# Optimization experiments

Hardware: AMD Instinct MI355X
Metric: run time of the kernel (lower is better)

## Reference

```python
import jax, jax.numpy as jnp
import numpy as np

N, E, G = 50000, 800000, 64          # nodes, edges, graphs in batch
H, C = 4, 32                          # heads, per-head channels
D = H * C                             # 128 = gat_hidden_dim * n_heads
EMB = 16
IN_DIM = 2 * EMB + 1                  # 33
LSTM_H = 256
OUT = 4
V_LAB, V_TYP = 1000, 100
EPS = 1e-5


def _gatv2(x, src, dst, Wl, bl, Wr, br, att, bias):
    # GATv2Conv (PyG semantics, self-loops already appended to src/dst).
    xl = (x @ Wl + bl).reshape(-1, H, C)   # lin_l -> source-side messages x_j
    xr = (x @ Wr + br).reshape(-1, H, C)   # lin_r -> target-side x_i
    xj = xl[src]                            # [Et, H, C]
    e = jax.nn.leaky_relu(xr[dst] + xj, 0.2)
    score = jnp.einsum('ehc,hc->eh', e, att)             # [Et, H]
    smax = jax.ops.segment_max(score, dst, num_segments=N)
    a = jnp.exp(score - smax[dst])
    denom = jax.ops.segment_sum(a, dst, num_segments=N)
    alpha = a / denom[dst]                                # scatter-softmax per dst
    out = jax.ops.segment_sum(xj * alpha[:, :, None], dst, num_segments=N)
    return out.reshape(N, D) + bias


def _graph_norm(x, batch_ids, w, b, ms):
    # PyG GraphNorm: per-graph mean (scaled by learnable ms) and variance.
    cnt = jax.ops.segment_sum(jnp.ones((N,), x.dtype), batch_ids, num_segments=G)[:, None]
    mean = jax.ops.segment_sum(x, batch_ids, num_segments=G) / cnt
    out = x - mean[batch_ids] * ms
    var = jax.ops.segment_sum(out * out, batch_ids, num_segments=G) / cnt
    return w * out / jnp.sqrt(var + EPS)[batch_ids] + b


def _lstm0(x, Wih, Whh, bih, bhh):
    # Single LSTM time-step with h0 = c0 = 0: the Whh @ h0 term vanishes,
    # the forget gate multiplies c0 = 0.  Gate order (PyTorch): i, f, g, o.
    g = x @ Wih.T + bih + bhh
    i, f, gg, o = jnp.split(g, 4, axis=-1)
    c = jax.nn.sigmoid(i) * jnp.tanh(gg)
    return jax.nn.sigmoid(o) * jnp.tanh(c)


def setup_inputs() -> dict:
    key = jax.random.key(0)
    ks = jax.random.split(key, 32)
    rn = lambda k, s, sc=0.05: jax.random.normal(k, s, jnp.float32) * sc
    Z4 = LSTM_H * 4
    return {
        'node_labels': jax.random.randint(ks[0], (N,), 0, V_LAB, jnp.int32),
        'node_types': jax.random.randint(ks[1], (N,), 0, V_TYP, jnp.int32),
        'node_feat': jax.random.normal(ks[2], (N, 1), jnp.float32),
        'edge_index': jax.random.randint(ks[3], (2, E), 0, N, jnp.int32),
        'batch_ids': jnp.sort(jax.random.randint(ks[4], (N,), 0, G, jnp.int32)),
        'emb_label': rn(ks[5], (V_LAB, EMB), 1.0),
        'emb_type': rn(ks[6], (V_TYP, EMB), 1.0),
        'W_in': rn(ks[7], (IN_DIM, D)), 'b_in': jnp.zeros((D,), jnp.float32),
        'g1_Wl': rn(ks[8], (D, D)), 'g1_bl': jnp.zeros((D,), jnp.float32),
        'g1_Wr': rn(ks[9], (D, D)), 'g1_br': jnp.zeros((D,), jnp.float32),
        'g1_att': rn(ks[10], (H, C), 0.1), 'g1_bias': jnp.zeros((D,), jnp.float32),
        'gn1_w': jnp.ones((D,), jnp.float32), 'gn1_b': jnp.zeros((D,), jnp.float32),
        'gn1_ms': jnp.ones((D,), jnp.float32),
        'g2_Wl': rn(ks[11], (D, D)), 'g2_bl': jnp.zeros((D,), jnp.float32),
        'g2_Wr': rn(ks[12], (D, D)), 'g2_br': jnp.zeros((D,), jnp.float32),
        'g2_att': rn(ks[13], (H, C), 0.1), 'g2_bias': jnp.zeros((D,), jnp.float32),
        'gn2_w': jnp.ones((D,), jnp.float32), 'gn2_b': jnp.zeros((D,), jnp.float32),
        'gn2_ms': jnp.ones((D,), jnp.float32),
        'W_res': rn(ks[14], (D, D)), 'b_res': jnp.zeros((D,), jnp.float32),
        'l1_Wih': rn(ks[15], (Z4, D)), 'l1_Whh': rn(ks[16], (Z4, LSTM_H)),
        'l1_bih': jnp.zeros((Z4,), jnp.float32), 'l1_bhh': jnp.zeros((Z4,), jnp.float32),
        'l2_Wih': rn(ks[17], (Z4, LSTM_H)), 'l2_Whh': rn(ks[18], (Z4, LSTM_H)),
        'l2_bih': jnp.zeros((Z4,), jnp.float32), 'l2_bhh': jnp.zeros((Z4,), jnp.float32),
        'ln_w': jnp.ones((LSTM_H,), jnp.float32), 'ln_b': jnp.zeros((LSTM_H,), jnp.float32),
        'fc_W': rn(ks[19], (LSTM_H, OUT)), 'fc_b': jnp.zeros((OUT,), jnp.float32),
    }


def reference(node_labels, node_types, node_feat, edge_index, batch_ids,
              emb_label, emb_type, W_in, b_in,
              g1_Wl, g1_bl, g1_Wr, g1_br, g1_att, g1_bias, gn1_w, gn1_b, gn1_ms,
              g2_Wl, g2_bl, g2_Wr, g2_br, g2_att, g2_bias, gn2_w, gn2_b, gn2_ms,
              W_res, b_res,
              l1_Wih, l1_Whh, l1_bih, l1_bhh, l2_Wih, l2_Whh, l2_bih, l2_bhh,
              ln_w, ln_b, fc_W, fc_b):
    # Node features: [label_emb | type_emb | scalar]  -> [N, 33]
    feat = jnp.concatenate([emb_label[node_labels], emb_type[node_types], node_feat], axis=1)
    # PositionalEncoding at position 0 with odd d_model=33 adds exactly zeros (no-op).
    x = feat @ W_in + b_in                                  # [N, D]

    loops = jnp.arange(N, dtype=edge_index.dtype)           # GATv2Conv add_self_loops=True
    src = jnp.concatenate([edge_index[0], loops])
    dst = jnp.concatenate([edge_index[1], loops])

    x1 = jax.nn.elu(_graph_norm(_gatv2(x, src, dst, g1_Wl, g1_bl, g1_Wr, g1_br, g1_att, g1_bias),
                                batch_ids, gn1_w, gn1_b, gn1_ms))
    # dropout = identity in eval mode
    x2 = jax.nn.elu(_graph_norm(_gatv2(x1, src, dst, g2_Wl, g2_bl, g2_Wr, g2_br, g2_att, g2_bias),
                                batch_ids, gn2_w, gn2_b, gn2_ms) + x1 @ W_res + b_res)

    h1 = _lstm0(x2, l1_Wih, l1_Whh, l1_bih, l1_bhh)         # seq_len = 1 LSTM
    h2 = _lstm0(h1, l2_Wih, l2_Whh, l2_bih, l2_bhh)

    mu = h2.mean(-1, keepdims=True)
    var = ((h2 - mu) ** 2).mean(-1, keepdims=True)
    hn = ln_w * (h2 - mu) / jnp.sqrt(var + EPS) + ln_b      # LayerNorm

    cnt = jax.ops.segment_sum(jnp.ones((N,), hn.dtype), batch_ids, num_segments=G)[:, None]
    pooled = jax.ops.segment_sum(hn, batch_ids, num_segments=G) / cnt  # global_mean_pool
    return jax.nn.log_softmax(pooled @ fc_W + fc_b, axis=1)            # [G, OUT]
```

## Files before the change

kernel.cpp:

```cpp
#include <hip/hip_runtime.h>
#include <cstdint>
#include <cstddef>

#define DD 128
#define LSTMH 256
#define ZG 1024

typedef __attribute__((ext_vector_type(8))) short short8v;
typedef __attribute__((ext_vector_type(4))) float float4v;

static inline int cdiv_(int a, int b) { return (a + b - 1) / b; }

__device__ __forceinline__ float sigm_(float x) { return 1.f / (1.f + __expf(-x)); }
__device__ __forceinline__ float tanh_(float x) {
  float e = __expf(-2.f * fabsf(x));
  float r = (1.f - e) / (1.f + e);
  return copysignf(r, x);
}

__device__ __forceinline__ unsigned short f2bf(float f) {
  uint32_t u = __float_as_uint(f);
  u += 0x7fffu + ((u >> 16) & 1u);
  return (unsigned short)(u >> 16);
}
__device__ __forceinline__ float bflo(uint32_t u) { return __uint_as_float(u << 16); }
__device__ __forceinline__ float bfhi(uint32_t u) { return __uint_as_float(u & 0xffff0000u); }
__device__ __forceinline__ float bfu(unsigned short u) { return __uint_as_float((uint32_t)u << 16); }

__global__ void cvt_direct(const float* __restrict__ W, unsigned short* __restrict__ o, int n) {
  int i = blockIdx.x * 256 + threadIdx.x;
  if (i < n) o[i] = f2bf(W[i]);
}

__global__ void cvt_transpose(const float* __restrict__ W, unsigned short* __restrict__ o,
                              int K, int M) {
  int i = blockIdx.x * 256 + threadIdx.x;
  if (i >= K * M) return;
  int m = i / K, k = i - m * K;
  o[i] = f2bf(W[(size_t)k * M + m]);
}

__global__ void prep_small(const float* g1bl, const float* g1br, const float* g2bl,
                           const float* g2br, const float* bres, const float* l1bih,
                           const float* l1bhh, const float* l2bih, const float* l2bhh,
                           float* bcat1, float* bcat2, float* bsum1, float* bsum2) {
  int t = blockIdx.x * 256 + threadIdx.x;
  if (t < 256) bcat1[t] = t < 128 ? g1bl[t] : g1br[t - 128];
  if (t < 384) bcat2[t] = t < 128 ? g2bl[t] : (t < 256 ? g2br[t - 128] : bres[t - 256]);
  if (t < ZG) { bsum1[t] = l1bih[t] + l1bhh[t]; bsum2[t] = l2bih[t] + l2bhh[t]; }
}

__global__ __launch_bounds__(128) void embed_in(
    const int* __restrict__ labels, const int* __restrict__ types,
    const float* __restrict__ nf, const float* __restrict__ embL,
    const float* __restrict__ embT, const float* __restrict__ W,
    const float* __restrict__ b, unsigned short* __restrict__ x, int N) {
  int n = blockIdx.x;
  if (n >= N) return;
  int t = threadIdx.x;
  __shared__ float f[33];
  if (t < 16) f[t] = embL[labels[n] * 16 + t];
  else if (t < 32) f[t] = embT[types[n] * 16 + (t - 16)];
  else if (t == 32) f[32] = nf[n];
  __syncthreads();
  float acc = b[t];
#pragma unroll
  for (int k = 0; k < 33; ++k) acc += f[k] * W[k * DD + t];
  x[(size_t)n * DD + t] = f2bf(acc);
}

__global__ void count_deg(const int* __restrict__ ei, int* __restrict__ deg, int E_, int N_) {
  int i = blockIdx.x * 256 + threadIdx.x;
  if (i < E_) atomicAdd(&deg[ei[E_ + i]], 1);
  else if (i < E_ + N_) atomicAdd(&deg[i - E_], 1);
}

__global__ __launch_bounds__(256) void scan1(const int* __restrict__ deg, int* __restrict__ offs,
                                             int* __restrict__ partials, int N_) {
  __shared__ int buf[2][256];
  int tid = threadIdx.x;
  int i = blockIdx.x * 256 + tid;
  int v = (i < N_) ? deg[i] : 0;
  buf[0][tid] = v;
  __syncthreads();
  int cur = 0;
#pragma unroll
  for (int d = 1; d < 256; d <<= 1) {
    int xv = buf[cur][tid];
    if (tid >= d) xv += buf[cur][tid - d];
    buf[cur ^ 1][tid] = xv;
    cur ^= 1;
    __syncthreads();
  }
  int incl = buf[cur][tid];
  if (i < N_) offs[i] = incl - v;
  if (tid == 255) partials[blockIdx.x] = incl;
}

__global__ __launch_bounds__(256) void scan2(int* __restrict__ partials, int* __restrict__ offs,
                                             int nb, int N_) {
  __shared__ int buf[2][256];
  int tid = threadIdx.x;
  int v = (tid < nb) ? partials[tid] : 0;
  buf[0][tid] = v;
  __syncthreads();
  int cur = 0;
#pragma unroll
  for (int d = 1; d < 256; d <<= 1) {
    int xv = buf[cur][tid];
    if (tid >= d) xv += buf[cur][tid - d];
    buf[cur ^ 1][tid] = xv;
    cur ^= 1;
    __syncthreads();
  }
  int incl = buf[cur][tid];
  if (tid < nb) partials[tid] = incl - v;
  if (tid == 255) offs[N_] = incl;
}

__global__ void scan3(int* __restrict__ offs, const int* __restrict__ partials, int N_) {
  int i = blockIdx.x * 256 + threadIdx.x;
  if (i < N_) offs[i] += partials[blockIdx.x];
}

__global__ void fill_csr(const int* __restrict__ ei, const int* __restrict__ offs,
                         int* __restrict__ cursor, int* __restrict__ csr, int E_, int N_) {
  int i = blockIdx.x * 256 + threadIdx.x;
  int s, d;
  if (i < E_) { s = ei[i]; d = ei[E_ + i]; }
  else if (i < E_ + N_) { s = d = i - E_; }
  else return;
  int pos = offs[d] + atomicAdd(&cursor[d], 1);
  csr[pos] = s;
}

__global__ void graph_ranges(const int* __restrict__ bids, int* __restrict__ gstart,
                             float* __restrict__ invcnt, int N_, int G_) {
  int t = threadIdx.x;
  if (t <= G_) {
    int lo = 0, hi = N_;
    while (lo < hi) { int mid = (lo + hi) >> 1; if (bids[mid] < t) lo = mid + 1; else hi = mid; }
    gstart[t] = lo;
  }
  __syncthreads();
  if (t < G_) {
    int c = gstart[t + 1] - gstart[t];
    invcnt[t] = (c > 0) ? 1.f / (float)c : 0.f;
  }
}

__global__ __launch_bounds__(256) void gemm_bf16(
    const unsigned short* __restrict__ A, const unsigned short* __restrict__ Bp,
    const float* __restrict__ bias, unsigned short* __restrict__ C, int M, int K, int Ncols) {
  __shared__ unsigned short As[128 * 40];
  __shared__ unsigned short Bs[128 * 40];
  int tid = threadIdx.x;
  int lane = tid & 63;
  int wid = tid >> 6;
  int rowBase = blockIdx.y * 128, colBase = blockIdx.x * 128;
  int wr = (wid >> 1) * 64, wc = (wid & 1) * 64;
  int fr = lane & 15, fg = lane >> 4;
  float4v acc[4][4];
#pragma unroll
  for (int i = 0; i < 4; ++i)
#pragma unroll
    for (int j = 0; j < 4; ++j) acc[i][j] = (float4v){0.f, 0.f, 0.f, 0.f};

  int sr = tid >> 2;
  int sc = tid & 3;
  int off_lo = (sc < 2) ? 32 * sc : 32 * sc - 56;

  for (int k0 = 0; k0 < K; k0 += 32) {
#pragma unroll
    for (int it = 0; it < 2; ++it) {
      int r = it * 64 + sr;
      uint4 va = make_uint4(0u, 0u, 0u, 0u);
      if (rowBase + r < M)
        va = *(const uint4*)(A + (size_t)(rowBase + r) * K + k0 + sc * 8);
      char* arow = (char*)(As + r * 40);
      *(uint2*)(arow + off_lo) = make_uint2(va.x, va.y);
      *(uint2*)(arow + off_lo + 16) = make_uint2(va.z, va.w);
      uint4 vb = *(const uint4*)(Bp + (size_t)(colBase + r) * K + k0 + sc * 8);
      char* brow = (char*)(Bs + r * 40);
      *(uint2*)(brow + off_lo) = make_uint2(vb.x, vb.y);
      *(uint2*)(brow + off_lo + 16) = make_uint2(vb.z, vb.w);
    }
    __syncthreads();
    short8v af[4], bfv[4];
#pragma unroll
    for (int i = 0; i < 4; ++i)
      af[i] = *(const short8v*)((const char*)As + (wr + 16 * i + fr) * 80 + fg * 16);
#pragma unroll
    for (int j = 0; j < 4; ++j)
      bfv[j] = *(const short8v*)((const char*)Bs + (wc + 16 * j + fr) * 80 + fg * 16);
#pragma unroll
    for (int i = 0; i < 4; ++i)
#pragma unroll
      for (int j = 0; j < 4; ++j)
        acc[i][j] = __builtin_amdgcn_mfma_f32_16x16x32_bf16(af[i], bfv[j], acc[i][j], 0, 0, 0);
    __syncthreads();
  }
#pragma unroll
  for (int j = 0; j < 4; ++j) {
    int gc = colBase + wc + 16 * j + fr;
    float bv = bias[gc];
#pragma unroll
    for (int i = 0; i < 4; ++i) {
      int gr0 = rowBase + wr + 16 * i + fg * 4;
#pragma unroll
      for (int rg = 0; rg < 4; ++rg) {
        int gr = gr0 + rg;
        if (gr < M) C[(size_t)gr * Ncols + gc] = f2bf(acc[i][j][rg] + bv);
      }
    }
  }
}

__global__ __launch_bounds__(256) void gat_agg(
    const unsigned short* __restrict__ xlr, int stride,
    const int* __restrict__ csr, const int* __restrict__ offs,
    const float* __restrict__ att, const float* __restrict__ bias,
    float* __restrict__ out, int N) {
  int wid = (blockIdx.x * 256 + threadIdx.x) >> 6;
  if (wid >= N) return;
  int lane = threadIdx.x & 63;
  int q = lane >> 4, ql = lane & 15;
  float4 aA = *(const float4*)&att[ql * 8];
  float4 aB = *(const float4*)&att[ql * 8 + 4];
  uint4 ur = *(const uint4*)(xlr + (size_t)wid * stride + 128 + ql * 8);
  float r0 = bflo(ur.x), r1 = bfhi(ur.x), r2 = bflo(ur.y), r3 = bfhi(ur.y);
  float r4 = bflo(ur.z), r5 = bfhi(ur.z), r6 = bflo(ur.w), r7 = bfhi(ur.w);
  float m = -1e30f, L = 0.f;
  float s0 = 0.f, s1 = 0.f, s2 = 0.f, s3 = 0.f, s4 = 0.f, s5 = 0.f, s6 = 0.f, s7 = 0.f;
  int js = offs[wid], je = offs[wid + 1];
  for (int j = js + q; j < je; j += 4) {
    int s = csr[j];
    uint4 u = *(const uint4*)(xlr + (size_t)s * stride + ql * 8);
    float x0 = bflo(u.x), x1 = bfhi(u.x), x2 = bflo(u.y), x3 = bfhi(u.y);
    float x4 = bflo(u.z), x5 = bfhi(u.z), x6 = bflo(u.w), x7 = bfhi(u.w);
    float v0 = fmaxf(r0 + x0, 0.2f * (r0 + x0));
    float v1 = fmaxf(r1 + x1, 0.2f * (r1 + x1));
    float v2 = fmaxf(r2 + x2, 0.2f * (r2 + x2));
    float v3 = fmaxf(r3 + x3, 0.2f * (r3 + x3));
    float v4 = fmaxf(r4 + x4, 0.2f * (r4 + x4));
    float v5 = fmaxf(r5 + x5, 0.2f * (r5 + x5));
    float v6 = fmaxf(r6 + x6, 0.2f * (r6 + x6));
    float v7 = fmaxf(r7 + x7, 0.2f * (r7 + x7));
    float p = aA.x * v0 + aA.y * v1 + aA.z * v2 + aA.w * v3 +
              aB.x * v4 + aB.y * v5 + aB.z * v6 + aB.w * v7;
    p += __shfl_xor(p, 1); p += __shfl_xor(p, 2);
    p += __shfl_xor(p, 4); p += __shfl_xor(p, 8);
    float mn = fmaxf(m, p);
    float ea = __expf(p - mn);
    float es = __expf(m - mn);
    L = L * es + ea;
    s0 = s0 * es + ea * x0; s1 = s1 * es + ea * x1;
    s2 = s2 * es + ea * x2; s3 = s3 * es + ea * x3;
    s4 = s4 * es + ea * x4; s5 = s5 * es + ea * x5;
    s6 = s6 * es + ea * x6; s7 = s7 * es + ea * x7;
    m = mn;
  }
#pragma unroll
  for (int d = 16; d <= 32; d <<= 1) {
    float mo = __shfl_xor(m, d), Lo = __shfl_xor(L, d);
    float t0 = __shfl_xor(s0, d), t1 = __shfl_xor(s1, d);
    float t2 = __shfl_xor(s2, d), t3 = __shfl_xor(s3, d);
    float t4 = __shfl_xor(s4, d), t5 = __shfl_xor(s5, d);
    float t6 = __shfl_xor(s6, d), t7 = __shfl_xor(s7, d);
    float mn = fmaxf(m, mo);
    float e0 = __expf(m - mn), e1 = __expf(mo - mn);
    L = L * e0 + Lo * e1;
    s0 = s0 * e0 + t0 * e1; s1 = s1 * e0 + t1 * e1;
    s2 = s2 * e0 + t2 * e1; s3 = s3 * e0 + t3 * e1;
    s4 = s4 * e0 + t4 * e1; s5 = s5 * e0 + t5 * e1;
    s6 = s6 * e0 + t6 * e1; s7 = s7 * e0 + t7 * e1;
    m = mn;
  }
  if (q == 0) {
    float inv = 1.f / L;
    float4 bA = *(const float4*)&bias[ql * 8];
    float4 bB = *(const float4*)&bias[ql * 8 + 4];
    float4 oA, oB;
    oA.x = s0 * inv + bA.x; oA.y = s1 * inv + bA.y;
    oA.z = s2 * inv + bA.z; oA.w = s3 * inv + bA.w;
    oB.x = s4 * inv + bB.x; oB.y = s5 * inv + bB.y;
    oB.z = s6 * inv + bB.z; oB.w = s7 * inv + bB.w;
    *(float4*)&out[(size_t)wid * DD + ql * 8] = oA;
    *(float4*)&out[(size_t)wid * DD + ql * 8 + 4] = oB;
  }
}

__global__ __launch_bounds__(256) void gn_stats2(const float* __restrict__ x,
                                                 const int* __restrict__ bids,
                                                 float* __restrict__ gsum,
                                                 float* __restrict__ gsq, int N) {
  int base = blockIdx.x * 128;
  int ch = threadIdx.x & 127;
  int sub = threadIdx.x >> 7;
  int end = base + 128 < N ? base + 128 : N;
  int curg = -1;
  float s = 0.f, q = 0.f;
  for (int r = base + sub; r < end; r += 2) {
    int g = bids[r];
    if (g != curg) {
      if (curg >= 0) {
        atomicAdd(&gsum[curg * DD + ch], s);
        atomicAdd(&gsq[curg * DD + ch], q);
      }
      curg = g; s = 0.f; q = 0.f;
    }
    float v = x[(size_t)r * DD + ch];
    s += v; q += v * v;
  }
  if (curg >= 0) {
    atomicAdd(&gsum[curg * DD + ch], s);
    atomicAdd(&gsq[curg * DD + ch], q);
  }
}

template <bool ADDRES>
__global__ void gn_apply(const float* __restrict__ xin, unsigned short* __restrict__ xout,
                         const unsigned short* __restrict__ res, int resStride,
                         const int* __restrict__ bids, const float* __restrict__ gsum,
                         const float* __restrict__ gsq, const float* __restrict__ invcnt,
                         const float* __restrict__ w, const float* __restrict__ b,
                         const float* __restrict__ ms, int N) {
  int idx = blockIdx.x * 256 + threadIdx.x;
  if (idx >= N * DD) return;
  int n = idx >> 7, ch = idx & 127;
  int g = bids[n];
  float ic = invcnt[g];
  float mean = gsum[g * DD + ch] * ic;
  float ex2 = gsq[g * DD + ch] * ic;
  float mm = mean * ms[ch];
  float var = ex2 - mm * (2.f * mean - mm);
  float v = (xin[idx] - mm) * rsqrtf(var + 1e-5f) * w[ch] + b[ch];
  if (ADDRES) v += bfu(res[(size_t)n * resStride + ch]);
  v = v > 0.f ? v : (__expf(v) - 1.f);
  xout[idx] = f2bf(v);
}

template <int KD>
__global__ __launch_bounds__(512, 4) void lstm_big(
    const unsigned short* __restrict__ A, const unsigned short* __restrict__ Bp,
    const float* __restrict__ bsum, unsigned short* __restrict__ H, int M) {
  __shared__ __attribute__((aligned(16))) char As_[128 * 272];
  __shared__ __attribute__((aligned(16))) char Ws_[96 * 272];
  const int NPH = KD / 128;
  int npanel = (M + 127) >> 7;
  int b = blockIdx.x;
  int g8 = b & 7, inner = b >> 3;
  int p = g8 + 8 * (inner >> 3);
  int cc = inner & 7;
  if (p >= npanel) return;
  int rowBase = p << 7;
  int ch0 = cc * 32;

  int tid = threadIdx.x;
  int lane = tid & 63;
  int wid = tid >> 6;
  int wr4 = wid >> 1;
  int wc2 = wid & 1;
  int fr = lane & 15, fg = lane >> 4;

  int ar[4], ac[4], aolo[4], aldst[4];
#pragma unroll
  for (int q = 0; q < 4; ++q) {
    int e = q * 512 + tid;
    int r = e >> 4, kk = e & 15;
    int c = kk >> 2, sc = kk & 3;
    ar[q] = r; ac[q] = c;
    aolo[q] = (sc < 2) ? 32 * sc : 32 * sc - 56;
    aldst[q] = r * 272 + c * 64;
  }
  int wgrow[3], wc_[3], wolo[3], wldst[3];
#pragma unroll
  for (int q = 0; q < 3; ++q) {
    int e = q * 512 + tid;
    int wrow = e >> 4, kk = e & 15;
    int c = kk >> 2, sc = kk & 3;
    int half = wrow >= 48 ? 1 : 0;
    int r3 = wrow - 48 * half;
    int grp = r3 >> 4;
    int goff = (grp == 0) ? 0 : (grp == 1 ? 512 : 768);
    wgrow[q] = goff + ch0 + 16 * half + (r3 & 15);
    wc_[q] = c;
    wolo[q] = (sc < 2) ? 32 * sc : 32 * sc - 56;
    wldst[q] = wrow * 272 + c * 64;
  }

  float4v acc[2][3];
#pragma unroll
  for (int i = 0; i < 2; ++i)
#pragma unroll
    for (int j = 0; j < 3; ++j) acc[i][j] = (float4v){0.f, 0.f, 0.f, 0.f};

  uint4 va[4], vw[3];
#pragma unroll
  for (int q = 0; q < 4; ++q) {
    va[q] = make_uint4(0u, 0u, 0u, 0u);
    if (rowBase + ar[q] < M)
      va[q] = *(const uint4*)(A + (size_t)(rowBase + ar[q]) * KD + ac[q] * 32 + (aolo[q] == 32 || aolo[q] == 40 ? 0 : 0) + ((aolo[q] < 32) ? (aolo[q] >> 5) * 0 : 0) + 0 + ((q * 512 + tid) & 3) * 8);
  }
#pragma unroll
  for (int q = 0; q < 4; ++q) {
    int e = q * 512 + tid;
    int sc = e & 3;
    va[q] = make_uint4(0u, 0u, 0u, 0u);
    if (rowBase + ar[q] < M)
      va[q] = *(const uint4*)(A + (size_t)(rowBase + ar[q]) * KD + ac[q] * 32 + sc * 8);
  }
#pragma unroll
  for (int q = 0; q < 3; ++q) {
    int e = q * 512 + tid;
    int sc = e & 3;
    vw[q] = *(const uint4*)(Bp + (size_t)wgrow[q] * KD + wc_[q] * 32 + sc * 8);
  }

#pragma unroll
  for (int ph = 0; ph < NPH; ++ph) {
    if (ph) __syncthreads();
#pragma unroll
    for (int q = 0; q < 4; ++q) {
      char* dst = As_ + aldst[q];
      *(uint2*)(dst + aolo[q]) = make_uint2(va[q].x, va[q].y);
      *(uint2*)(dst + aolo[q] + 16) = make_uint2(va[q].z, va[q].w);
    }
#pragma unroll
    for (int q = 0; q < 3; ++q) {
      char* dst = Ws_ + wldst[q];
      *(uint2*)(dst + wolo[q]) = make_uint2(vw[q].x, vw[q].y);
      *(uint2*)(dst + wolo[q] + 16) = make_uint2(vw[q].z, vw[q].w);
    }
    __syncthreads();
    if (ph + 1 < NPH) {
      int koff = (ph + 1) * 128;
#pragma unroll
      for (int q = 0; q < 4; ++q) {
        int e = q * 512 + tid;
        int sc = e & 3;
        va[q] = make_uint4(0u, 0u, 0u, 0u);
        if (rowBase + ar[q] < M)
          va[q] = *(const uint4*)(A + (size_t)(rowBase + ar[q]) * KD + koff + ac[q] * 32 + sc * 8);
      }
#pragma unroll
      for (int q = 0; q < 3; ++q) {
        int e = q * 512 + tid;
        int sc = e & 3;
        vw[q] = *(const uint4*)(Bp + (size_t)wgrow[q] * KD + koff + wc_[q] * 32 + sc * 8);
      }
    }
#pragma unroll
    for (int c = 0; c < 4; ++c) {
      short8v af[2], bf[3];
#pragma unroll
      for (int i = 0; i < 2; ++i)
        af[i] = *(const short8v*)(As_ + (32 * wr4 + 16 * i + fr) * 272 + c * 64 + fg * 16);
#pragma unroll
      for (int j = 0; j < 3; ++j)
        bf[j] = *(const short8v*)(Ws_ + (48 * wc2 + 16 * j + fr) * 272 + c * 64 + fg * 16);
#pragma unroll
      for (int i = 0; i < 2; ++i)
#pragma unroll
        for (int j = 0; j < 3; ++j)
          acc[i][j] = __builtin_amdgcn_mfma_f32_16x16x32_bf16(af[i], bf[j], acc[i][j], 0, 0, 0);
    }
  }
  int chL = 16 * wc2 + fr;
  int ch = ch0 + chL;
  float bi = bsum[ch], bg = bsum[512 + ch], bo = bsum[768 + ch];
  unsigned short hv[8];
#pragma unroll
  for (int i = 0; i < 2; ++i) {
#pragma unroll
    for (int rg = 0; rg < 4; ++rg) {
      float iv = acc[i][0][rg] + bi;
      float gv = acc[i][1][rg] + bg;
      float ov = acc[i][2][rg] + bo;
      float c = sigm_(iv) * tanh_(gv);
      hv[i * 4 + rg] = f2bf(sigm_(ov) * tanh_(c));
    }
  }
  __syncthreads();
  unsigned short* Hs = (unsigned short*)As_;
#pragma unroll
  for (int i = 0; i < 2; ++i) {
#pragma unroll
    for (int rg = 0; rg < 4; ++rg) {
      int row = 32 * wr4 + 16 * i + 4 * fg + rg;
      Hs[row * 40 + chL] = hv[i * 4 + rg];
    }
  }
  __syncthreads();
  {
    int row = tid >> 2, seg = tid & 3;
    if (rowBase + row < M) {
      uint4 v = *(const uint4*)(Hs + row * 40 + seg * 8);
      *(uint4*)(H + (size_t)(rowBase + row) * LSTMH + ch0 + seg * 8) = v;
    }
  }
}

__global__ __launch_bounds__(256) void ln_pool2(
    const unsigned short* __restrict__ h2, const int* __restrict__ bids,
    const float* __restrict__ lnw, const float* __restrict__ lnb,
    const float* __restrict__ invcnt, float* __restrict__ pooled, int N) {
  int wave = (blockIdx.x * 256 + threadIdx.x) >> 6;
  int lane = threadIdx.x & 63;
  int r0 = wave * 8;
  if (r0 >= N) return;
  float4 w4 = *(const float4*)&lnw[lane * 4];
  float4 b4 = *(const float4*)&lnb[lane * 4];
  float p0 = 0.f, p1 = 0.f, p2 = 0.f, p3 = 0.f;
  int curg = bids[r0];
  int rend = r0 + 8 < N ? r0 + 8 : N;
  for (int r = r0; r < rend; ++r) {
    int g = bids[r];
    if (g != curg) {
      float ic = invcnt[curg];
      atomicAdd(&pooled[curg * LSTMH + lane * 4 + 0], p0 * ic);
      atomicAdd(&pooled[curg * LSTMH + lane * 4 + 1], p1 * ic);
      atomicAdd(&pooled[curg * LSTMH + lane * 4 + 2], p2 * ic);
      atomicAdd(&pooled[curg * LSTMH + lane * 4 + 3], p3 * ic);
      p0 = p1 = p2 = p3 = 0.f;
      curg = g;
    }
    uint2 u = *(const uint2*)(h2 + (size_t)r * LSTMH + lane * 4);
    float v0 = bflo(u.x), v1 = bfhi(u.x), v2 = bflo(u.y), v3 = bfhi(u.y);
    float s = v0 + v1 + v2 + v3;
    float q = v0 * v0 + v1 * v1 + v2 * v2 + v3 * v3;
#pragma unroll
    for (int d = 1; d < 64; d <<= 1) { s += __shfl_xor(s, d); q += __shfl_xor(q, d); }
    float mu = s * (1.f / 256.f);
    float var = q * (1.f / 256.f) - mu * mu;
    float rs = rsqrtf(var + 1e-5f);
    p0 += w4.x * (v0 - mu) * rs + b4.x;
    p1 += w4.y * (v1 - mu) * rs + b4.y;
    p2 += w4.z * (v2 - mu) * rs + b4.z;
    p3 += w4.w * (v3 - mu) * rs + b4.w;
  }
  float ic = invcnt[curg];
  atomicAdd(&pooled[curg * LSTMH + lane * 4 + 0], p0 * ic);
  atomicAdd(&pooled[curg * LSTMH + lane * 4 + 1], p1 * ic);
  atomicAdd(&pooled[curg * LSTMH + lane * 4 + 2], p2 * ic);
  atomicAdd(&pooled[curg * LSTMH + lane * 4 + 3], p3 * ic);
}

__global__ __launch_bounds__(64) void fc_lsm(const float* __restrict__ pooled,
                                             const float* __restrict__ W,
                                             const float* __restrict__ b, float* __restrict__ out) {
  int g = blockIdx.x;
  int t = threadIdx.x;
  float l0 = 0.f, l1 = 0.f, l2 = 0.f, l3 = 0.f;
  for (int k = t; k < LSTMH; k += 64) {
    float p = pooled[g * LSTMH + k];
    l0 += p * W[k * 4 + 0];
    l1 += p * W[k * 4 + 1];
    l2 += p * W[k * 4 + 2];
    l3 += p * W[k * 4 + 3];
  }
#pragma unroll
  for (int d = 1; d < 64; d <<= 1) {
    l0 += __shfl_xor(l0, d); l1 += __shfl_xor(l1, d);
    l2 += __shfl_xor(l2, d); l3 += __shfl_xor(l3, d);
  }
  if (t == 0) {
    float z[4] = {l0 + b[0], l1 + b[1], l2 + b[2], l3 + b[3]};
    float mx = fmaxf(fmaxf(z[0], z[1]), fmaxf(z[2], z[3]));
    float sum = __expf(z[0] - mx) + __expf(z[1] - mx) + __expf(z[2] - mx) + __expf(z[3] - mx);
    float ls = logf(sum);
#pragma unroll
    for (int o = 0; o < 4; ++o) out[g * 4 + o] = z[o] - mx - ls;
  }
}

extern "C" void kernel_launch(void* const* d_in, const int* in_sizes, int n_in,
                              void* d_out, int out_size, void* d_ws, size_t ws_size,
                              hipStream_t stream) {
  const int* node_labels = (const int*)d_in[0];
  const int* node_types = (const int*)d_in[1];
  const float* node_feat = (const float*)d_in[2];
  const int* edge_index = (const int*)d_in[3];
  const int* batch_ids = (const int*)d_in[4];
  const float* emb_label = (const float*)d_in[5];
  const float* emb_type = (const float*)d_in[6];
  const float* W_in = (const float*)d_in[7];
  const float* b_in = (const float*)d_in[8];
  const float* g1_Wl = (const float*)d_in[9];
  const float* g1_bl = (const float*)d_in[10];
  const float* g1_Wr = (const float*)d_in[11];
  const float* g1_br = (const float*)d_in[12];
  const float* g1_att = (const float*)d_in[13];
  const float* g1_bias = (const float*)d_in[14];
  const float* gn1_w = (const float*)d_in[15];
  const float* gn1_b = (const float*)d_in[16];
  const float* gn1_ms = (const float*)d_in[17];
  const float* g2_Wl = (const float*)d_in[18];
  const float* g2_bl = (const float*)d_in[19];
  const float* g2_Wr = (const float*)d_in[20];
  const float* g2_br = (const float*)d_in[21];
  const float* g2_att = (const float*)d_in[22];
  const float* g2_bias = (const float*)d_in[23];
  const float* gn2_w = (const float*)d_in[24];
  const float* gn2_b = (const float*)d_in[25];
  const float* gn2_ms = (const float*)d_in[26];
  const float* W_res = (const float*)d_in[27];
  const float* b_res = (const float*)d_in[28];
  const float* l1_Wih = (const float*)d_in[29];
  const float* l1_bih = (const float*)d_in[31];
  const float* l1_bhh = (const float*)d_in[32];
  const float* l2_Wih = (const float*)d_in[33];
  const float* l2_bih = (const float*)d_in[35];
  const float* l2_bhh = (const float*)d_in[36];
  const float* ln_w = (const float*)d_in[37];
  const float* ln_b = (const float*)d_in[38];
  const float* fc_W = (const float*)d_in[39];
  const float* fc_b = (const float*)d_in[40];
  float* out = (float*)d_out;

  const int N = in_sizes[0];
  const int E = in_sizes[3] / 2;
  const int G = out_size / 4;
  const int ET = E + N;

  char* wsb = (char*)d_ws;
  size_t off = 0;
  auto alloc = [&](size_t bytes) -> void* {
    void* p = (void*)(wsb + off);
    off = (off + bytes + 255) & ~(size_t)255;
    return p;
  };
  float* xA = (float*)alloc((size_t)N * DD * 4);
  unsigned short* xb = (unsigned short*)alloc((size_t)N * DD * 2);
  unsigned short* xlr = (unsigned short*)alloc((size_t)N * 384 * 2);
  int* deg = (int*)alloc((size_t)N * 4);
  int* offs = (int*)alloc((size_t)(N + 1) * 4);
  int* cursor = (int*)alloc((size_t)N * 4);
  int* partials = (int*)alloc(1024);
  int* csr = (int*)alloc((size_t)ET * 4);
  int* gstart = (int*)alloc((size_t)(G + 1) * 4);
  float* invcnt = (float*)alloc((size_t)G * 4);
  float* gsum = (float*)alloc((size_t)G * DD * 4);
  float* gsq = (float*)alloc((size_t)G * DD * 4);
  float* pooled = (float*)alloc((size_t)G * LSTMH * 4);
  float* bcat1 = (float*)alloc(256 * 4);
  float* bcat2 = (float*)alloc(384 * 4);
  float* bsum1 = (float*)alloc(ZG * 4);
  float* bsum2 = (float*)alloc(ZG * 4);
  unsigned short* wcat1 = (unsigned short*)alloc((size_t)256 * DD * 2);
  unsigned short* wcat2 = (unsigned short*)alloc((size_t)384 * DD * 2);
  unsigned short* wl1b = (unsigned short*)alloc((size_t)ZG * DD * 2);
  unsigned short* wl2b = (unsigned short*)alloc((size_t)ZG * LSTMH * 2);
  (void)ws_size; (void)n_in;

  unsigned short* h1 = xlr;
  unsigned short* h2 = (unsigned short*)xA;

  hipMemsetAsync(deg, 0, (size_t)N * 4, stream);
  hipMemsetAsync(cursor, 0, (size_t)N * 4, stream);
  hipMemsetAsync(pooled, 0, (size_t)G * LSTMH * 4, stream);

  cvt_transpose<<<cdiv_(DD * DD, 256), 256, 0, stream>>>(g1_Wl, wcat1, DD, DD);
  cvt_transpose<<<cdiv_(DD * DD, 256), 256, 0, stream>>>(g1_Wr, wcat1 + DD * DD, DD, DD);
  cvt_transpose<<<cdiv_(DD * DD, 256), 256, 0, stream>>>(g2_Wl, wcat2, DD, DD);
  cvt_transpose<<<cdiv_(DD * DD, 256), 256, 0, stream>>>(g2_Wr, wcat2 + DD * DD, DD, DD);
  cvt_transpose<<<cdiv_(DD * DD, 256), 256, 0, stream>>>(W_res, wcat2 + 2 * DD * DD, DD, DD);
  cvt_direct<<<cdiv_(ZG * DD, 256), 256, 0, stream>>>(l1_Wih, wl1b, ZG * DD);
  cvt_direct<<<cdiv_(ZG * LSTMH, 256), 256, 0, stream>>>(l2_Wih, wl2b, ZG * LSTMH);
  prep_small<<<4, 256, 0, stream>>>(g1_bl, g1_br, g2_bl, g2_br, b_res, l1_bih, l1_bhh,
                                    l2_bih, l2_bhh, bcat1, bcat2, bsum1, bsum2);

  graph_ranges<<<1, 128, 0, stream>>>(batch_ids, gstart, invcnt, N, G);
  embed_in<<<N, 128, 0, stream>>>(node_labels, node_types, node_feat, emb_label, emb_type,
                                  W_in, b_in, xb, N);

  count_deg<<<cdiv_(ET, 256), 256, 0, stream>>>(edge_index, deg, E, N);
  int nb1 = cdiv_(N, 256);
  scan1<<<nb1, 256, 0, stream>>>(deg, offs, partials, N);
  scan2<<<1, 256, 0, stream>>>(partials, offs, nb1, N);
  scan3<<<nb1, 256, 0, stream>>>(offs, partials, N);
  fill_csr<<<cdiv_(ET, 256), 256, 0, stream>>>(edge_index, offs, cursor, csr, E, N);

  int mb = cdiv_(N, 128);
  gemm_bf16<<<dim3(2, mb), 256, 0, stream>>>(xb, wcat1, bcat1, xlr, N, DD, 256);
  gat_agg<<<cdiv_(N, 4), 256, 0, stream>>>(xlr, 256, csr, offs, g1_att, g1_bias, xA, N);
  hipMemsetAsync(gsum, 0, (size_t)G * DD * 8, stream);
  gn_stats2<<<cdiv_(N, 128), 256, 0, stream>>>(xA, batch_ids, gsum, gsq, N);
  gn_apply<false><<<cdiv_(N * DD, 256), 256, 0, stream>>>(
      xA, xb, nullptr, 0, batch_ids, gsum, gsq, invcnt, gn1_w, gn1_b, gn1_ms, N);
  gemm_bf16<<<dim3(3, mb), 256, 0, stream>>>(xb, wcat2, bcat2, xlr, N, DD, 384);
  gat_agg<<<cdiv_(N, 4), 256, 0, stream>>>(xlr, 384, csr, offs, g2_att, g2_bias, xA, N);
  hipMemsetAsync(gsum, 0, (size_t)G * DD * 8, stream);
  gn_stats2<<<cdiv_(N, 128), 256, 0, stream>>>(xA, batch_ids, gsum, gsq, N);
  gn_apply<true><<<cdiv_(N * DD, 256), 256, 0, stream>>>(
      xA, xb, xlr + 256, 384, batch_ids, gsum, gsq, invcnt, gn2_w, gn2_b, gn2_ms, N);
  int npanel = cdiv_(N, 128);
  int lblocks = 64 * cdiv_(npanel, 8);
  lstm_big<DD><<<lblocks, 512, 0, stream>>>(xb, wl1b, bsum1, h1, N);
  lstm_big<LSTMH><<<lblocks, 512, 0, stream>>>(h1, wl2b, bsum2, h2, N);
  ln_pool2<<<cdiv_(N, 32), 256, 0, stream>>>(h2, batch_ids, ln_w, ln_b, invcnt, pooled, N);
  fc_lsm<<<G, 64, 0, stream>>>(pooled, fc_W, fc_b, out);
}
```

Before: 533.6 us.

## Fuse prep kernels, tile embedding, store GAT output as bf16, vectorize GraphNorm

Merges seven weight/bias preparation launches into one kernel. The input embedding now handles 128 nodes per block with the 33 weight rows kept in registers, replacing one block per node. The GAT aggregation output becomes bf16 instead of fp32, and the GraphNorm stats/apply kernels read it two channels at a time, which roughly halves that intermediate traffic at some precision cost. The attention score reduction now sums only within each head's 4 lanes, which corrects the old code that summed across all heads; the GEMM also gains s_setprio around its MFMA loop and redundant loads are removed.

After: 487.0 us. -8.7%, faster.

```diff
diff --git a/kernel.cpp b/kernel.cpp
--- a/kernel.cpp
+++ b/kernel.cpp
@@ -23,50 +23,78 @@
   u += 0x7fffu + ((u >> 16) & 1u);
   return (unsigned short)(u >> 16);
 }
+__device__ __forceinline__ uint32_t bfpack(float a, float b) {
+  return (uint32_t)f2bf(a) | ((uint32_t)f2bf(b) << 16);
+}
 __device__ __forceinline__ float bflo(uint32_t u) { return __uint_as_float(u << 16); }
 __device__ __forceinline__ float bfhi(uint32_t u) { return __uint_as_float(u & 0xffff0000u); }
-__device__ __forceinline__ float bfu(unsigned short u) { return __uint_as_float((uint32_t)u << 16); }
-
-__global__ void cvt_direct(const float* __restrict__ W, unsigned short* __restrict__ o, int n) {
+
+__global__ void prep_all(const float* __restrict__ g1Wl, const float* __restrict__ g1Wr,
+                         const float* __restrict__ g2Wl, const float* __restrict__ g2Wr,
+                         const float* __restrict__ Wres, const float* __restrict__ l1Wih,
+                         const float* __restrict__ l2Wih, const float* __restrict__ g1bl,
+                         const float* __restrict__ g1br, const float* __restrict__ g2bl,
+                         const float* __restrict__ g2br, const float* __restrict__ bres,
+                         const float* __restrict__ l1bih, const float* __restrict__ l1bhh,
+                         const float* __restrict__ l2bih, const float* __restrict__ l2bhh,
+                         unsigned short* __restrict__ wcat1, unsigned short* __restrict__ wcat2,
+                         unsigned short* __restrict__ wl1b, unsigned short* __restrict__ wl2b,
+                         float* __restrict__ bcat1, float* __restrict__ bcat2,
+                         float* __restrict__ bsum1, float* __restrict__ bsum2) {
   int i = blockIdx.x * 256 + threadIdx.x;
-  if (i < n) o[i] = f2bf(W[i]);
-}
-
-__global__ void cvt_transpose(const float* __restrict__ W, unsigned short* __restrict__ o,
-                              int K, int M) {
-  int i = blockIdx.x * 256 + threadIdx.x;
-  if (i >= K * M) return;
-  int m = i / K, k = i - m * K;
-  o[i] = f2bf(W[(size_t)k * M + m]);
-}
-
-__global__ void prep_small(const float* g1bl, const float* g1br, const float* g2bl,
-                           const float* g2br, const float* bres, const float* l1bih,
-                           const float* l1bhh, const float* l2bih, const float* l2bhh,
-                           float* bcat1, float* bcat2, float* bsum1, float* bsum2) {
-  int t = blockIdx.x * 256 + threadIdx.x;
-  if (t < 256) bcat1[t] = t < 128 ? g1bl[t] : g1br[t - 128];
-  if (t < 384) bcat2[t] = t < 128 ? g2bl[t] : (t < 256 ? g2br[t - 128] : bres[t - 256]);
-  if (t < ZG) { bsum1[t] = l1bih[t] + l1bhh[t]; bsum2[t] = l2bih[t] + l2bhh[t]; }
-}
-
-__global__ __launch_bounds__(128) void embed_in(
+  if (i < 81920) {
+    int seg = i >> 14, j = i & 16383;
+    int m = j >> 7, k = j & 127;
+    const float* src = (seg == 0) ? g1Wl : (seg == 1) ? g1Wr : (seg == 2) ? g2Wl
+                       : (seg == 3) ? g2Wr : Wres;
+    unsigned short* dst = (seg == 0) ? wcat1 : (seg == 1) ? wcat1 + 16384
+                          : (seg == 2) ? wcat2 : (seg == 3) ? wcat2 + 16384 : wcat2 + 32768;
+    dst[j] = f2bf(src[k * 128 + m]);
+    return;
+  }
+  i -= 81920;
+  if (i < 131072) { wl1b[i] = f2bf(l1Wih[i]); return; }
+  i -= 131072;
+  if (i < 262144) { wl2b[i] = f2bf(l2Wih[i]); return; }
+  i -= 262144;
+  if (i < 256) { bcat1[i] = (i < 128) ? g1bl[i] : g1br[i - 128]; return; }
+  i -= 256;
+  if (i < 384) {
+    bcat2[i] = (i < 128) ? g2bl[i] : (i < 256 ? g2br[i - 128] : bres[i - 256]);
+    return;
+  }
+  i -= 384;
+  if (i < 1024) { bsum1[i] = l1bih[i] + l1bhh[i]; return; }
+  i -= 1024;
+  if (i < 1024) { bsum2[i] = l2bih[i] + l2bhh[i]; return; }
+}
+
+__global__ __launch_bounds__(256) void embed_in2(
     const int* __restrict__ labels, const int* __restrict__ types,
     const float* __restrict__ nf, const float* __restrict__ embL,
     const float* __restrict__ embT, const float* __restrict__ W,
     const float* __restrict__ b, unsigned short* __restrict__ x, int N) {
-  int n = blockIdx.x;
-  if (n >= N) return;
-  int t = threadIdx.x;
-  __shared__ float f[33];
-  if (t < 16) f[t] = embL[labels[n] * 16 + t];
-  else if (t < 32) f[t] = embT[types[n] * 16 + (t - 16)];
-  else if (t == 32) f[32] = nf[n];
+  __shared__ float f[128][34];
+  int base = blockIdx.x * 128;
+  int tid = threadIdx.x;
+  int ch = tid & 127, half = tid >> 7;
+  float wr[33];
+#pragma unroll
+  for (int k = 0; k < 33; ++k) wr[k] = W[k * 128 + ch];
+  float bb = b[ch];
+  int nmax = N - base < 128 ? N - base : 128;
+  for (int e = tid; e < nmax * 32; e += 256) {
+    int n = e >> 5, k = e & 31;
+    f[n][k] = (k < 16) ? embL[labels[base + n] * 16 + k] : embT[types[base + n] * 16 + (k - 16)];
+  }
+  for (int n = tid; n < nmax; n += 256) f[n][32] = nf[base + n];
   __syncthreads();
-  float acc = b[t];
-#pragma unroll
-  for (int k = 0; k < 33; ++k) acc += f[k] * W[k * DD + t];
-  x[(size_t)n * DD + t] = f2bf(acc);
+  for (int n = half; n < nmax; n += 2) {
+    float acc = bb;
+#pragma unroll
+    for (int k = 0; k < 33; ++k) acc = fmaf(f[n][k], wr[k], acc);
+    x[(size_t)(base + n) * 128 + ch] = f2bf(acc);
+  }
 }
 
 __global__ void count_deg(const int* __restrict__ ei, int* __restrict__ deg, int E_, int N_) {
@@ -220,7 +248,7 @@
     const unsigned short* __restrict__ xlr, int stride,
     const int* __restrict__ csr, const int* __restrict__ offs,
     const float* __restrict__ att, const float* __restrict__ bias,
-    float* __restrict__ out, int N) {
+    unsigned short* __restrict__ out, int N) {
   int wid = (blockIdx.x * 256 + threadIdx.x) >> 6;
   if (wid >= N) return;
   int lane = threadIdx.x & 63;
@@ -249,7 +277,6 @@
     float p = aA.x * v0 + aA.y * v1 + aA.z * v2 + aA.w * v3 +
               aB.x * v4 + aB.y * v5 + aB.z * v6 + aB.w * v7;
     p += __shfl_xor(p, 1); p += __shfl_xor(p, 2);
-    p += __shfl_xor(p, 4); p += __shfl_xor(p, 8);
     float mn = fmaxf(m, p);
     float ea = __expf(p - mn);
     float es = __expf(m - mn);
@@ -280,64 +307,80 @@
     float inv = 1.f / L;
     float4 bA = *(const float4*)&bias[ql * 8];
     float4 bB = *(const float4*)&bias[ql * 8 + 4];
-    float4 oA, oB;
-    oA.x = s0 * inv + bA.x; oA.y = s1 * inv + bA.y;
-    oA.z = s2 * inv + bA.z; oA.w = s3 * inv + bA.w;
-    oB.x = s4 * inv + bB.x; oB.y = s5 * inv + bB.y;
-    oB.z = s6 * inv + bB.z; oB.w = s7 * inv + bB.w;
-    *(float4*)&out[(size_t)wid * DD + ql * 8] = oA;
-    *(float4*)&out[(size_t)wid * DD + ql * 8 + 4] = oB;
-  }
-}
-
-__global__ __launch_bounds__(256) void gn_stats2(const float* __restrict__ x,
+    uint4 ov;
+    ov.x = bfpack(s0 * inv + bA.x, s1 * inv + bA.y);
+    ov.y = bfpack(s2 * inv + bA.z, s3 * inv + bA.w);
+    ov.z = bfpack(s4 * inv + bB.x, s5 * inv + bB.y);
+    ov.w = bfpack(s6 * inv + bB.z, s7 * inv + bB.w);
+    *(uint4*)(out + (size_t)wid * DD + ql * 8) = ov;
+  }
+}
+
+__global__ __launch_bounds__(256) void gn_stats2(const unsigned short* __restrict__ x,
                                                  const int* __restrict__ bids,
                                                  float* __restrict__ gsum,
                                                  float* __restrict__ gsq, int N) {
   int base = blockIdx.x * 128;
-  int ch = threadIdx.x & 127;
-  int sub = threadIdx.x >> 7;
+  int cp = threadIdx.x & 63;
+  int sub = threadIdx.x >> 6;
   int end = base + 128 < N ? base + 128 : N;
   int curg = -1;
-  float s = 0.f, q = 0.f;
-  for (int r = base + sub; r < end; r += 2) {
+  float s0 = 0.f, s1 = 0.f, q0 = 0.f, q1 = 0.f;
+  for (int r = base + sub; r < end; r += 4) {
     int g = bids[r];
     if (g != curg) {
       if (curg >= 0) {
-        atomicAdd(&gsum[curg * DD + ch], s);
-        atomicAdd(&gsq[curg * DD + ch], q);
+        atomicAdd(&gsum[curg * DD + cp * 2], s0);
+        atomicAdd(&gsum[curg * DD + cp * 2 + 1], s1);
+        atomicAdd(&gsq[curg * DD + cp * 2], q0);
+        atomicAdd(&gsq[curg * DD + cp * 2 + 1], q1);
       }
-      curg = g; s = 0.f; q = 0.f;
-    }
-    float v = x[(size_t)r * DD + ch];
-    s += v; q += v * v;
+      curg = g; s0 = s1 = q0 = q1 = 0.f;
+    }
+    uint32_t u = *(const uint32_t*)(x + (size_t)r * DD + cp * 2);
+    float v0 = bflo(u), v1 = bfhi(u);
+    s0 += v0; q0 += v0 * v0; s1 += v1; q1 += v1 * v1;
   }
   if (curg >= 0) {
-    atomicAdd(&gsum[curg * DD + ch], s);
-    atomicAdd(&gsq[curg * DD + ch], q);
+    atomicAdd(&gsum[curg * DD + cp * 2], s0);
+    atomicAdd(&gsum[curg * DD + cp * 2 + 1], s1);
+    atomicAdd(&gsq[curg * DD + cp * 2], q0);
+    atomicAdd(&gsq[curg * DD + cp * 2 + 1], q1);
   }
 }
 
 template <bool ADDRES>
-__global__ void gn_apply(const float* __restrict__ xin, unsigned short* __restrict__ xout,
+__global__ void gn_apply(const unsigned short* __restrict__ xin,
+                         unsigned short* __restrict__ xout,
                          const unsigned short* __restrict__ res, int resStride,
                          const int* __restrict__ bids, const float* __restrict__ gsum,
                          const float* __restrict__ gsq, const float* __restrict__ invcnt,
                          const float* __restrict__ w, const float* __restrict__ b,
                          const float* __restrict__ ms, int N) {
   int idx = blockIdx.x * 256 + threadIdx.x;
-  if (idx >= N * DD) return;
-  int n = idx >> 7, ch = idx & 127;
+  if (idx >= N * 64) return;
+  int n = idx >> 6, cp = idx & 63;
   int g = bids[n];
   float ic = invcnt[g];
-  float mean = gsum[g * DD + ch] * ic;
-  float ex2 = gsq[g * DD + ch] * ic;
-  float mm = mean * ms[ch];
-  float var = ex2 - mm * (2.f * mean - mm);
-  float v = (xin[idx] - mm) * rsqrtf(var + 1e-5f) * w[ch] + b[ch];
-  if (ADDRES) v += bfu(res[(size_t)n * resStride + ch]);
-  v = v > 0.f ? v : (__expf(v) - 1.f);
-  xout[idx] = f2bf(v);
+  float2 sm = *(const float2*)&gsum[g * DD + cp * 2];
+  float2 sq = *(const float2*)&gsq[g * DD + cp * 2];
+  float2 w2 = *(const float2*)&w[cp * 2];
+  float2 b2 = *(const float2*)&b[cp * 2];
+  float2 m2 = *(const float2*)&ms[cp * 2];
+  uint32_t u = *(const uint32_t*)(xin + (size_t)n * DD + cp * 2);
+  float mean0 = sm.x * ic, mean1 = sm.y * ic;
+  float mm0 = mean0 * m2.x, mm1 = mean1 * m2.y;
+  float var0 = sq.x * ic - mm0 * (2.f * mean0 - mm0);
+  float var1 = sq.y * ic - mm1 * (2.f * mean1 - mm1);
+  float v0 = (bflo(u) - mm0) * rsqrtf(var0 + 1e-5f) * w2.x + b2.x;
+  float v1 = (bfhi(u) - mm1) * rsqrtf(var1 + 1e-5f) * w2.y + b2.y;
+  if (ADDRES) {
+    uint32_t ur = *(const uint32_t*)(res + (size_t)n * resStride + cp * 2);
+    v0 += bflo(ur); v1 += bfhi(ur);
+  }
+  v0 = v0 > 0.f ? v0 : (__expf(v0) - 1.f);
+  v1 = v1 > 0.f ? v1 : (__expf(v1) - 1.f);
+  *(uint32_t*)(xout + (size_t)n * DD + cp * 2) = bfpack(v0, v1);
 }
 
 template <int KD>
@@ -363,17 +406,17 @@
   int wc2 = wid & 1;
   int fr = lane & 15, fg = lane >> 4;
 
-  int ar[4], ac[4], aolo[4], aldst[4];
+  int ar[4], ac[4], asc[4], aolo[4], aldst[4];
 #pragma unroll
   for (int q = 0; q < 4; ++q) {
     int e = q * 512 + tid;
     int r = e >> 4, kk = e & 15;
     int c = kk >> 2, sc = kk & 3;
-    ar[q] = r; ac[q] = c;
+    ar[q] = r; ac[q] = c; asc[q] = sc;
     aolo[q] = (sc < 2) ? 32 * sc : 32 * sc - 56;
     aldst[q] = r * 272 + c * 64;
   }
-  int wgrow[3], wc_[3], wolo[3], wldst[3];
+  int wgrow[3], wc_[3], wsc[3], wolo[3], wldst[3];
 #pragma unroll
   for (int q = 0; q < 3; ++q) {
     int e = q * 512 + tid;
@@ -384,7 +427,7 @@
     int grp = r3 >> 4;
     int goff = (grp == 0) ? 0 : (grp == 1 ? 512 : 768);
     wgrow[q] = goff + ch0 + 16 * half + (r3 & 15);
-    wc_[q] = c;
+    wc_[q] = c; wsc[q] = sc;
     wolo[q] = (sc < 2) ? 32 * sc : 32 * sc - 56;
     wldst[q] = wrow * 272 + c * 64;
   }
@@ -400,22 +443,11 @@
   for (int q = 0; q < 4; ++q) {
     va[q] = make_uint4(0u, 0u, 0u, 0u);
     if (rowBase + ar[q] < M)
-      va[q] = *(const uint4*)(A + (size_t)(rowBase + ar[q]) * KD + ac[q] * 32 + (aolo[q] == 32 || aolo[q] == 40 ? 0 : 0) + ((aolo[q] < 32) ? (aolo[q] >> 5) * 0 : 0) + 0 + ((q * 512 + tid) & 3) * 8);
-  }
-#pragma unroll
-  for (int q = 0; q < 4; ++q) {
-    int e = q * 512 + tid;
-    int sc = e & 3;
-    va[q] = make_uint4(0u, 0u, 0u, 0u);
-    if (rowBase + ar[q] < M)
-      va[q] = *(const uint4*)(A + (size_t)(rowBase + ar[q]) * KD + ac[q] * 32 + sc * 8);
-  }
-#pragma unroll
-  for (int q = 0; q < 3; ++q) {
-    int e = q * 512 + tid;
-    int sc = e & 3;
-    vw[q] = *(const uint4*)(Bp + (size_t)wgrow[q] * KD + wc_[q] * 32 + sc * 8);
-  }
+      va[q] = *(const uint4*)(A + (size_t)(rowBase + ar[q]) * KD + ac[q] * 32 + asc[q] * 8);
+  }
+#pragma unroll
+  for (int q = 0; q < 3; ++q)
+    vw[q] = *(const uint4*)(Bp + (size_t)wgrow[q] * KD + wc_[q] * 32 + wsc[q] * 8);
 
 #pragma unroll
   for (int ph = 0; ph < NPH; ++ph) {
@@ -437,19 +469,15 @@
       int koff = (ph + 1) * 128;
 #pragma unroll
       for (int q = 0; q < 4; ++q) {
-        int e = q * 512 + tid;
-        int sc = e & 3;
         va[q] = make_uint4(0u, 0u, 0u, 0u);
         if (rowBase + ar[q] < M)
-          va[q] = *(const uint4*)(A + (size_t)(rowBase + ar[q]) * KD + koff + ac[q] * 32 + sc * 8);
+          va[q] = *(const uint4*)(A + (size_t)(rowBase + ar[q]) * KD + koff + ac[q] * 32 + asc[q] * 8);
       }
 #pragma unroll
-      for (int q = 0; q < 3; ++q) {
-        int e = q * 512 + tid;
-        int sc = e & 3;
-        vw[q] = *(const uint4*)(Bp + (size_t)wgrow[q] * KD + koff + wc_[q] * 32 + sc * 8);
-      }
-    }
+      for (int q = 0; q < 3; ++q)
+        vw[q] = *(const uint4*)(Bp + (size_t)wgrow[q] * KD + koff + wc_[q] * 32 + wsc[q] * 8);
+    }
+    __builtin_amdgcn_s_setprio(1);
 #pragma unroll
     for (int c = 0; c < 4; ++c) {
       short8v af[2], bf[3];
@@ -465,6 +493,7 @@
         for (int j = 0; j < 3; ++j)
           acc[i][j] = __builtin_amdgcn_mfma_f32_16x16x32_bf16(af[i], bf[j], acc[i][j], 0, 0, 0);
     }
+    __builtin_amdgcn_s_setprio(0);
   }
   int chL = 16 * wc2 + fr;
   int ch = ch0 + chL;
@@ -630,7 +659,7 @@
     off = (off + bytes + 255) & ~(size_t)255;
     return p;
   };
-  float* xA = (float*)alloc((size_t)N * DD * 4);
+  unsigned short* xA = (unsigned short*)alloc((size_t)N * 512);
   unsigned short* xb = (unsigned short*)alloc((size_t)N * DD * 2);
   unsigned short* xlr = (unsigned short*)alloc((size_t)N * 384 * 2);
   int* deg = (int*)alloc((size_t)N * 4);
@@ -654,25 +683,19 @@
   (void)ws_size; (void)n_in;
 
   unsigned short* h1 = xlr;
-  unsigned short* h2 = (unsigned short*)xA;
+  unsigned short* h2 = xA;
 
   hipMemsetAsync(deg, 0, (size_t)N * 4, stream);
   hipMemsetAsync(cursor, 0, (size_t)N * 4, stream);
   hipMemsetAsync(pooled, 0, (size_t)G * LSTMH * 4, stream);
 
-  cvt_transpose<<<cdiv_(DD * DD, 256), 256, 0, stream>>>(g1_Wl, wcat1, DD, DD);
-  cvt_transpose<<<cdiv_(DD * DD, 256), 256, 0, stream>>>(g1_Wr, wcat1 + DD * DD, DD, DD);
-  cvt_transpose<<<cdiv_(DD * DD, 256), 256, 0, stream>>>(g2_Wl, wcat2, DD, DD);
-  cvt_transpose<<<cdiv_(DD * DD, 256), 256, 0, stream>>>(g2_Wr, wcat2 + DD * DD, DD, DD);
-  cvt_transpose<<<cdiv_(DD * DD, 256), 256, 0, stream>>>(W_res, wcat2 + 2 * DD * DD, DD, DD);
-  cvt_direct<<<cdiv_(ZG * DD, 256), 256, 0, stream>>>(l1_Wih, wl1b, ZG * DD);
-  cvt_direct<<<cdiv_(ZG * LSTMH, 256), 256, 0, stream>>>(l2_Wih, wl2b, ZG * LSTMH);
-  prep_small<<<4, 256, 0, stream>>>(g1_bl, g1_br, g2_bl, g2_br, b_res, l1_bih, l1_bhh,
-                                    l2_bih, l2_bhh, bcat1, bcat2, bsum1, bsum2);
-
+  prep_all<<<1867, 256, 0, stream>>>(g1_Wl, g1_Wr, g2_Wl, g2_Wr, W_res, l1_Wih, l2_Wih,
+                                     g1_bl, g1_br, g2_bl, g2_br, b_res, l1_bih, l1_bhh,
+                                     l2_bih, l2_bhh, wcat1, wcat2, wl1b, wl2b,
+                                     bcat1, bcat2, bsum1, bsum2);
   graph_ranges<<<1, 128, 0, stream>>>(batch_ids, gstart, invcnt, N, G);
-  embed_in<<<N, 128, 0, stream>>>(node_labels, node_types, node_feat, emb_label, emb_type,
-                                  W_in, b_in, xb, N);
+  embed_in2<<<cdiv_(N, 128), 256, 0, stream>>>(node_labels, node_types, node_feat, emb_label,
+                                               emb_type, W_in, b_in, xb, N);
 
   count_deg<<<cdiv_(ET, 256), 256, 0, stream>>>(edge_index, deg, E, N);
   int nb1 = cdiv_(N, 256);
@@ -686,13 +709,13 @@
   gat_agg<<<cdiv_(N, 4), 256, 0, stream>>>(xlr, 256, csr, offs, g1_att, g1_bias, xA, N);
   hipMemsetAsync(gsum, 0, (size_t)G * DD * 8, stream);
   gn_stats2<<<cdiv_(N, 128), 256, 0, stream>>>(xA, batch_ids, gsum, gsq, N);
-  gn_apply<false><<<cdiv_(N * DD, 256), 256, 0, stream>>>(
+  gn_apply<false><<<cdiv_(N * 64, 256), 256, 0, stream>>>(
       xA, xb, nullptr, 0, batch_ids, gsum, gsq, invcnt, gn1_w, gn1_b, gn1_ms, N);
   gemm_bf16<<<dim3(3, mb), 256, 0, stream>>>(xb, wcat2, bcat2, xlr, N, DD, 384);
   gat_agg<<<cdiv_(N, 4), 256, 0, stream>>>(xlr, 384, csr, offs, g2_att, g2_bias, xA, N);
   hipMemsetAsync(gsum, 0, (size_t)G * DD * 8, stream);
   gn_stats2<<<cdiv_(N, 128), 256, 0, stream>>>(xA, batch_ids, gsum, gsq, N);
-  gn_apply<true><<<cdiv_(N * DD, 256), 256, 0, stream>>>(
+  gn_apply<true><<<cdiv_(N * 64, 256), 256, 0, stream>>>(
       xA, xb, xlr + 256, 384, batch_ids, gsum, gsq, invcnt, gn2_w, gn2_b, gn2_ms, N);
   int npanel = cdiv_(N, 128);
   int lblocks = 64 * cdiv_(npanel, 8);
```
